# Optimization experiments

Hardware: AMD Instinct MI355X
Metric: run time of the kernel (lower is better)

Reference implementation:

```python
import jax, jax.numpy as jnp
import numpy as np

STATE_DIM = 512
HIDDEN = 256
ACTION = 8
BATCH = 32768
LN_EPS = 1e-5


def setup_inputs() -> dict:
    key = jax.random.key(0)
    ks = jax.random.split(key, 24)
    s = 0.02
    inp = {
        'initial_state': jax.random.normal(ks[0], (BATCH, STATE_DIM), jnp.float32),
        'final_state': jax.random.normal(ks[1], (BATCH, STATE_DIM), jnp.float32),
        'horizon': 10,
        # fc: Linear(1024->256), LayerNorm(256), ReLU, Linear(256->256), ReLU
        'W1': jax.random.normal(ks[2], (HIDDEN, 2 * STATE_DIM), jnp.float32) * s,
        'b1': jnp.zeros((HIDDEN,), jnp.float32),
        'ln_g': jnp.ones((HIDDEN,), jnp.float32),
        'ln_b': jnp.zeros((HIDDEN,), jnp.float32),
        'W2': jax.random.normal(ks[3], (HIDDEN, HIDDEN), jnp.float32) * s,
        'b2': jnp.zeros((HIDDEN,), jnp.float32),
        # GRU layer 0 (input=ACTION) and layer 1 (input=HIDDEN)
        'Wih0': jax.random.normal(ks[4], (3 * HIDDEN, ACTION), jnp.float32) * s,
        'Whh0': jax.random.normal(ks[5], (3 * HIDDEN, HIDDEN), jnp.float32) * s,
        'bih0': jnp.zeros((3 * HIDDEN,), jnp.float32),
        'bhh0': jnp.zeros((3 * HIDDEN,), jnp.float32),
        'Wih1': jax.random.normal(ks[6], (3 * HIDDEN, HIDDEN), jnp.float32) * s,
        'Whh1': jax.random.normal(ks[7], (3 * HIDDEN, HIDDEN), jnp.float32) * s,
        'bih1': jnp.zeros((3 * HIDDEN,), jnp.float32),
        'bhh1': jnp.zeros((3 * HIDDEN,), jnp.float32),
        # fc_action: 256 -> 8
        'Wa': jax.random.normal(ks[8], (ACTION, HIDDEN), jnp.float32) * s,
        'ba': jnp.zeros((ACTION,), jnp.float32),
        # fc_init_hidden: 256 -> 512
        'Winit': jax.random.normal(ks[9], (2 * HIDDEN, HIDDEN), jnp.float32) * s,
        'binit': jnp.zeros((2 * HIDDEN,), jnp.float32),
    }
    return inp


def _gru_cell(x, h, Wih, Whh, bih, bhh):
    # torch.nn.GRU cell: gates ordered [r, z, n]
    gi = x @ Wih.T + bih              # [B, 3H]
    gh = h @ Whh.T + bhh              # [B, 3H]
    i_r, i_z, i_n = jnp.split(gi, 3, axis=-1)
    h_r, h_z, h_n = jnp.split(gh, 3, axis=-1)
    r = jax.nn.sigmoid(i_r + h_r)
    z = jax.nn.sigmoid(i_z + h_z)
    n = jnp.tanh(i_n + r * h_n)
    return (1.0 - z) * n + z * h


def reference(initial_state, final_state, horizon, W1, b1, ln_g, ln_b, W2, b2,
              Wih0, Whh0, bih0, bhh0, Wih1, Whh1, bih1, bhh1, Wa, ba, Winit, binit):
    B = initial_state.shape[0]
    combined = jnp.concatenate([initial_state, final_state], axis=-1)  # [B, 2*state]
    h = combined @ W1.T + b1
    mu = jnp.mean(h, axis=-1, keepdims=True)
    var = jnp.var(h, axis=-1, keepdims=True)
    h = (h - mu) * jax.lax.rsqrt(var + LN_EPS) * ln_g + ln_b
    h = jax.nn.relu(h)
    h = jax.nn.relu(h @ W2.T + b2)    # [B, H]

    # Replicates torch .view(2, B, H) on a [B, 2H] tensor (row-major reshape)
    hidden = jnp.reshape(h @ Winit.T + binit, (2, B, HIDDEN))
    h0, h1 = hidden[0], hidden[1]
    a0 = jnp.zeros((B, ACTION), initial_state.dtype)

    def step(carry, _):
        h0, h1, a = carry
        h0n = _gru_cell(a, h0, Wih0, Whh0, bih0, bhh0)
        h1n = _gru_cell(h0n, h1, Wih1, Whh1, bih1, bhh1)
        logits = h1n @ Wa.T + ba       # [B, A]
        a_next = jax.nn.softmax(logits, axis=-1)
        return (h0n, h1n, a_next), logits

    _, logits_seq = jax.lax.scan(step, (h0, h1, a0), None, length=horizon)
    return jnp.transpose(logits_seq, (1, 0, 2))  # [B, horizon, A]
```

## Files before the change

### kernel.cpp

```cpp
#include <hip/hip_runtime.h>


#define HS 264

typedef __attribute__((ext_vector_type(8))) short short8;
typedef __attribute__((ext_vector_type(4))) float fvec4;

__device__ __forceinline__ float bf2f(unsigned short u) {
    union { unsigned int u; float f; } x; x.u = ((unsigned int)u) << 16; return x.f;
}
__device__ __forceinline__ unsigned short f2bf(float f) {
    union { float f; unsigned int u; } x; x.f = f;
    unsigned int r = x.u + 0x7fffu + ((x.u >> 16) & 1u);
    return (unsigned short)(r >> 16);
}
__device__ __forceinline__ float sigm(float x)   { return __builtin_amdgcn_rcpf(1.f + __expf(-x)); }
__device__ __forceinline__ float tanh_f(float x) { return 2.f * __builtin_amdgcn_rcpf(1.f + __expf(-2.f * x)) - 1.f; }

__device__ __forceinline__ short8 ld8(const unsigned short* p) {
    return *reinterpret_cast<const short8*>(p);
}
__device__ __forceinline__ fvec4 mfma16(short8 a, short8 b, fvec4 c) {
    return __builtin_amdgcn_mfma_f32_16x16x32_bf16(a, b, c, 0, 0, 0);
}
__device__ __forceinline__ fvec4 splat4(float v) {
    fvec4 r = {v, v, v, v}; return r;
}

__device__ __forceinline__ int packoff(int e, int K) {
    const int n = e / K, k = e % K;
    return (((n >> 4) * (K >> 5) + (k >> 5)) << 9)
         + (((((k >> 3) & 3) << 4) | (n & 15)) << 3) + (k & 7);
}

__global__ __launch_bounds__(256) void k_prep(
    const float* __restrict__ W1, const float* __restrict__ W2,
    const float* __restrict__ Winit, const float* __restrict__ Wih0,
    const float* __restrict__ Whh0, const float* __restrict__ Wih1,
    const float* __restrict__ Whh1, const float* __restrict__ Wa,
    unsigned short* __restrict__ wb)
{
    int i = blockIdx.x * 256 + threadIdx.x;
    if (i >= 1056768) return;
    float v; int dst;
    if (i < 262144) {
        v = W1[i];                dst = packoff(i, 1024);
    } else if (i < 327680) {
        int e = i - 262144;  v = W2[e];    dst = 262144 + packoff(e, 256);
    } else if (i < 458752) {
        int e = i - 327680;  v = Winit[e]; dst = 327680 + packoff(e, 256);
    } else if (i < 464896) {
        v = Wih0[i - 458752];     dst = i;
    } else if (i < 661504) {
        int e = i - 464896;  v = Whh0[e];  dst = 464896 + packoff(e, 256);
    } else if (i < 858112) {
        int e = i - 661504;  v = Wih1[e];  dst = 661504 + packoff(e, 256);
    } else if (i < 1054720) {
        int e = i - 858112;  v = Whh1[e];  dst = 858112 + packoff(e, 256);
    } else {
        v = Wa[i - 1054720];      dst = i;
    }
    wb[dst] = f2bf(v);
}

__global__ __launch_bounds__(512, 2) void k_encode(
    const float* __restrict__ ini, const float* __restrict__ fin,
    const unsigned short* __restrict__ W1b, const float* __restrict__ b1,
    const float* __restrict__ lng, const float* __restrict__ lnb,
    const unsigned short* __restrict__ W2b, const float* __restrict__ b2,
    const unsigned short* __restrict__ Winitb, const float* __restrict__ binit,
    unsigned short* __restrict__ h0g, unsigned short* __restrict__ h1g)
{
    __shared__ unsigned short hb[64 * HS];
    __shared__ unsigned short at[2][64 * 40];
    __shared__ float ps[64][8][2];
    __shared__ float st[64][2];
    const int tid = threadIdx.x, lane = tid & 63, w = tid >> 6;
    const int l15 = lane & 15, q = lane >> 4;
    const int rows0 = blockIdx.x * 64;
    const int c0 = w * 32;
    const fvec4 fz = {0.f, 0.f, 0.f, 0.f};

    const int srow = tid >> 3, sseg = (tid & 7) * 4;

    fvec4 acc[4][2];
#pragma unroll
    for (int rt = 0; rt < 4; ++rt) { acc[rt][0] = fz; acc[rt][1] = fz; }
    {
        const float* src0 = ini + (rows0 + srow) * 512 + sseg;
        fvec4 v = *reinterpret_cast<const fvec4*>(src0);
        union { unsigned short s[4]; unsigned long long u; } p;
        p.s[0] = f2bf(v[0]); p.s[1] = f2bf(v[1]); p.s[2] = f2bf(v[2]); p.s[3] = f2bf(v[3]);
        *reinterpret_cast<unsigned long long*>(&at[0][srow * 40 + sseg]) = p.u;
    }
    __syncthreads();
#pragma unroll 1
    for (int kc = 0; kc < 32; ++kc) {
        const int buf = kc & 1;
        if (kc < 31) {
            const int k0 = (kc + 1) * 32 + sseg;
            const float* src = (k0 < 512) ? (ini + (rows0 + srow) * 512 + k0)
                                          : (fin + (rows0 + srow) * 512 + (k0 - 512));
            fvec4 v = *reinterpret_cast<const fvec4*>(src);
            union { unsigned short s[4]; unsigned long long u; } p;
            p.s[0] = f2bf(v[0]); p.s[1] = f2bf(v[1]); p.s[2] = f2bf(v[2]); p.s[3] = f2bf(v[3]);
            *reinterpret_cast<unsigned long long*>(&at[buf ^ 1][srow * 40 + sseg]) = p.u;
        }
        short8 b8a = ld8(W1b + (((w * 2 + 0) * 32 + kc) * 64 + lane) * 8);
        short8 b8b = ld8(W1b + (((w * 2 + 1) * 32 + kc) * 64 + lane) * 8);
        short8 a8[4];
#pragma unroll
        for (int rt = 0; rt < 4; ++rt)
            a8[rt] = ld8(&at[buf][(rt * 16 + l15) * 40 + q * 8]);
#pragma unroll
        for (int rt = 0; rt < 4; ++rt) {
            acc[rt][0] = mfma16(a8[rt], b8a, acc[rt][0]);
            acc[rt][1] = mfma16(a8[rt], b8b, acc[rt][1]);
        }
        __syncthreads();
    }
    float bv[2] = { b1[c0 + l15], b1[c0 + 16 + l15] };
#pragma unroll
    for (int rt = 0; rt < 4; ++rt)
#pragma unroll
        for (int r = 0; r < 4; ++r) {
            float s = 0.f, s2 = 0.f;
#pragma unroll
            for (int ct = 0; ct < 2; ++ct) {
                float v = acc[rt][ct][r] + bv[ct];
                acc[rt][ct][r] = v;
                s += v; s2 += v * v;
            }
#pragma unroll
            for (int off = 1; off < 16; off <<= 1) {
                s  += __shfl_xor(s,  off, 64);
                s2 += __shfl_xor(s2, off, 64);
            }
            if (l15 == 0) {
                int row = rt * 16 + q * 4 + r;
                ps[row][w][0] = s; ps[row][w][1] = s2;
            }
        }
    __syncthreads();
    if (tid < 64) {
        float s = 0.f, s2 = 0.f;
#pragma unroll
        for (int j = 0; j < 8; ++j) { s += ps[tid][j][0]; s2 += ps[tid][j][1]; }
        float mu = s * (1.f / 256.f);
        float var = s2 * (1.f / 256.f) - mu * mu;
        st[tid][0] = mu; st[tid][1] = rsqrtf(var + 1e-5f);
    }
    __syncthreads();
    {
        float gv[2]  = { lng[c0 + l15], lng[c0 + 16 + l15] };
        float bbv[2] = { lnb[c0 + l15], lnb[c0 + 16 + l15] };
#pragma unroll
        for (int rt = 0; rt < 4; ++rt)
#pragma unroll
            for (int ct = 0; ct < 2; ++ct)
#pragma unroll
                for (int r = 0; r < 4; ++r) {
                    int row = rt * 16 + q * 4 + r;
                    float v = (acc[rt][ct][r] - st[row][0]) * st[row][1] * gv[ct] + bbv[ct];
                    v = fmaxf(v, 0.f);
                    hb[row * HS + c0 + ct * 16 + l15] = f2bf(v);
                }
    }
    __syncthreads();
    fvec4 acc2[4][2];
#pragma unroll
    for (int rt = 0; rt < 4; ++rt) { acc2[rt][0] = fz; acc2[rt][1] = fz; }
#pragma unroll 2
    for (int kc = 0; kc < 8; ++kc) {
        const int k0 = kc * 32 + q * 8;
        short8 a8[4];
#pragma unroll
        for (int rt = 0; rt < 4; ++rt) a8[rt] = ld8(hb + (rt * 16 + l15) * HS + k0);
#pragma unroll
        for (int ct = 0; ct < 2; ++ct) {
            short8 b8 = ld8(W2b + (((w * 2 + ct) * 8 + kc) * 64 + lane) * 8);
#pragma unroll
            for (int rt = 0; rt < 4; ++rt) acc2[rt][ct] = mfma16(a8[rt], b8, acc2[rt][ct]);
        }
    }
    {
        float b2v[2] = { b2[c0 + l15], b2[c0 + 16 + l15] };
        unsigned short stg[4][2][4];
#pragma unroll
        for (int rt = 0; rt < 4; ++rt)
#pragma unroll
            for (int ct = 0; ct < 2; ++ct)
#pragma unroll
                for (int r = 0; r < 4; ++r)
                    stg[rt][ct][r] = f2bf(fmaxf(acc2[rt][ct][r] + b2v[ct], 0.f));
        __syncthreads();
#pragma unroll
        for (int rt = 0; rt < 4; ++rt)
#pragma unroll
            for (int ct = 0; ct < 2; ++ct)
#pragma unroll
                for (int r = 0; r < 4; ++r)
                    hb[(rt * 16 + q * 4 + r) * HS + c0 + ct * 16 + l15] = stg[rt][ct][r];
    }
    __syncthreads();
    fvec4 a3[4][4];
#pragma unroll
    for (int rt = 0; rt < 4; ++rt)
#pragma unroll
        for (int ct = 0; ct < 4; ++ct) a3[rt][ct] = fz;
#pragma unroll 1
    for (int kc = 0; kc < 8; ++kc) {
        const int k0 = kc * 32 + q * 8;
        short8 a8[4];
#pragma unroll
        for (int rt = 0; rt < 4; ++rt) a8[rt] = ld8(hb + (rt * 16 + l15) * HS + k0);
#pragma unroll
        for (int ct = 0; ct < 4; ++ct) {
            short8 b8 = ld8(Winitb + (((w * 4 + ct) * 8 + kc) * 64 + lane) * 8);
#pragma unroll
            for (int rt = 0; rt < 4; ++rt) a3[rt][ct] = mfma16(a8[rt], b8, a3[rt][ct]);
        }
    }
    const int c0i = w * 64;
#pragma unroll
    for (int ct = 0; ct < 4; ++ct) {
        const int j = c0i + ct * 16 + l15;
        const float bz = binit[j];
        const int half = j >> 8, cc = j & 255;
#pragma unroll
        for (int rt = 0; rt < 4; ++rt)
#pragma unroll
            for (int r = 0; r < 4; ++r) {
                const int i = rows0 + rt * 16 + q * 4 + r;
                const unsigned short v = f2bf(a3[rt][ct][r] + bz);
                if (i < 16384) h0g[(2 * i + half) * 256 + cc] = v;
                else           h1g[(2 * (i - 16384) + half) * 256 + cc] = v;
            }
    }
}

__global__ __launch_bounds__(512, 2) void k_roll(
    const unsigned short* __restrict__ h0g, const unsigned short* __restrict__ h1g,
    const unsigned short* __restrict__ Wih0b, const unsigned short* __restrict__ Whh0b,
    const unsigned short* __restrict__ Wih1b, const unsigned short* __restrict__ Whh1b,
    const unsigned short* __restrict__ Wab,
    const float* __restrict__ bih0, const float* __restrict__ bhh0,
    const float* __restrict__ bih1, const float* __restrict__ bhh1,
    const float* __restrict__ ba, float* __restrict__ out)
{
    __shared__ unsigned short h0sb[2][64 * HS];
    __shared__ unsigned short h1sb[2][64 * HS];
    __shared__ unsigned short avs[64 * 8];
    __shared__ float ldsb[2048];
    const int tid = threadIdx.x, lane = tid & 63, w = tid >> 6;
    const int l15 = lane & 15, q = lane >> 4;
    const int rows0 = blockIdx.x * 64;
    const int cb = w * 32;
    const fvec4 fz = {0.f, 0.f, 0.f, 0.f};
    const short8 z8 = {0,0,0,0,0,0,0,0};

    for (int it = tid; it < 64 * 32; it += 512) {
        const int row = it >> 5, g = (it & 31) * 8;
        *reinterpret_cast<short8*>(&h0sb[0][row * HS + g]) = ld8(h0g + (rows0 + row) * 256 + g);
        *reinterpret_cast<short8*>(&h1sb[0][row * HS + g]) = ld8(h1g + (rows0 + row) * 256 + g);
    }
    if (tid < 256) {
        const int j = tid;
        ldsb[j]       = bih0[j] + bhh0[j];
        ldsb[256 + j] = bih0[256 + j] + bhh0[256 + j];
        ldsb[512 + j] = bih0[512 + j];
        ldsb[768 + j] = bhh0[512 + j];
    } else {
        const int j = tid - 256;
        ldsb[1024 + j] = bih1[j] + bhh1[j];
        ldsb[1280 + j] = bih1[256 + j] + bhh1[256 + j];
        ldsb[1536 + j] = bih1[512 + j];
        ldsb[1792 + j] = bhh1[512 + j];
    }
    const float bav = ba[l15 & 7];
    __syncthreads();

    for (int t = 0; t < 10; ++t) {
        const int cur = t & 1, nxt = cur ^ 1;
        const unsigned short* h0c = h0sb[cur];
        unsigned short*       h0n = h0sb[nxt];
        const unsigned short* h1c = h1sb[cur];
        unsigned short*       h1n = h1sb[nxt];
        {
            fvec4 aR[4][2], aZ[4][2], aNi[4][2], aNh[4][2];
#pragma unroll
            for (int ct = 0; ct < 2; ++ct) {
                const int c = cb + ct * 16 + l15;
                const float vr = ldsb[c],       vz = ldsb[256 + c];
                const float vi = ldsb[512 + c], vh = ldsb[768 + c];
#pragma unroll
                for (int rt = 0; rt < 4; ++rt) {
                    aR[rt][ct]  = splat4(vr);
                    aZ[rt][ct]  = splat4(vz);
                    aNi[rt][ct] = splat4(vi);
                    aNh[rt][ct] = splat4(vh);
                }
            }
#pragma unroll 2
            for (int kc = 0; kc < 8; ++kc) {
                const int k0 = kc * 32 + q * 8;
                short8 wr[2], wz[2], wn[2];
#pragma unroll
                for (int ct = 0; ct < 2; ++ct) {
                    const unsigned short* wp =
                        Whh0b + ((((w * 2 + ct) * 8 + kc) * 64 + lane) * 8);
                    wr[ct] = ld8(wp);
                    wz[ct] = ld8(wp + 65536);
                    wn[ct] = ld8(wp + 131072);
                }
                short8 ah[4];
#pragma unroll
                for (int rt = 0; rt < 4; ++rt)
                    ah[rt] = ld8(h0c + (rt * 16 + l15) * HS + k0);
#pragma unroll
                for (int ct = 0; ct < 2; ++ct)
#pragma unroll
                    for (int rt = 0; rt < 4; ++rt) {
                        aR[rt][ct]  = mfma16(ah[rt], wr[ct], aR[rt][ct]);
                        aZ[rt][ct]  = mfma16(ah[rt], wz[ct], aZ[rt][ct]);
                        aNh[rt][ct] = mfma16(ah[rt], wn[ct], aNh[rt][ct]);
                    }
            }
            if (t > 0) {
                short8 av[4];
#pragma unroll
                for (int rt = 0; rt < 4; ++rt) {
                    short8 v = ld8(avs + (rt * 16 + l15) * 8);
                    av[rt] = (q == 0) ? v : z8;
                }
#pragma unroll
                for (int ct = 0; ct < 2; ++ct) {
                    const unsigned short* wp = Wih0b + (cb + ct * 16 + l15) * 8;
                    short8 wr = ld8(wp);
                    short8 wz = ld8(wp + 2048);
                    short8 wn = ld8(wp + 4096);
#pragma unroll
                    for (int rt = 0; rt < 4; ++rt) {
                        aR[rt][ct]  = mfma16(av[rt], wr, aR[rt][ct]);
                        aZ[rt][ct]  = mfma16(av[rt], wz, aZ[rt][ct]);
                        aNi[rt][ct] = mfma16(av[rt], wn, aNi[rt][ct]);
                    }
                }
            }
#pragma unroll
            for (int ct = 0; ct < 2; ++ct) {
                const int c = cb + ct * 16 + l15;
#pragma unroll
                for (int rt = 0; rt < 4; ++rt)
#pragma unroll
                    for (int r = 0; r < 4; ++r) {
                        const int row = rt * 16 + q * 4 + r;
                        const float hold = bf2f(h0c[row * HS + c]);
                        const float rr = sigm(aR[rt][ct][r]);
                        const float zz = sigm(aZ[rt][ct][r]);
                        const float nn = tanh_f(aNi[rt][ct][r] + rr * aNh[rt][ct][r]);
                        h0n[row * HS + c] = f2bf((1.f - zz) * nn + zz * hold);
                    }
            }
        }
        __syncthreads();
        {
            fvec4 aR[4][2], aZ[4][2], aNi[4][2], aNh[4][2];
#pragma unroll
            for (int ct = 0; ct < 2; ++ct) {
                const int c = cb + ct * 16 + l15;
                const float vr = ldsb[1024 + c], vz = ldsb[1280 + c];
                const float vi = ldsb[1536 + c], vh = ldsb[1792 + c];
#pragma unroll
                for (int rt = 0; rt < 4; ++rt) {
                    aR[rt][ct]  = splat4(vr);
                    aZ[rt][ct]  = splat4(vz);
                    aNi[rt][ct] = splat4(vi);
                    aNh[rt][ct] = splat4(vh);
                }
            }
#pragma unroll 1
            for (int kc = 0; kc < 8; ++kc) {
                const int k0 = kc * 32 + q * 8;
                short8 wir[2], wiz[2], win[2], whr[2], whz[2], whn[2];
#pragma unroll
                for (int ct = 0; ct < 2; ++ct) {
                    const int fo = (((w * 2 + ct) * 8 + kc) * 64 + lane) * 8;
                    const unsigned short* wi = Wih1b + fo;
                    const unsigned short* wh = Whh1b + fo;
                    wir[ct] = ld8(wi);
                    whr[ct] = ld8(wh);
                    wiz[ct] = ld8(wi + 65536);
                    whz[ct] = ld8(wh + 65536);
                    win[ct] = ld8(wi + 131072);
                    whn[ct] = ld8(wh + 131072);
                }
                short8 ai[4], ah[4];
#pragma unroll
                for (int rt = 0; rt < 4; ++rt) {
                    const int rr = (rt * 16 + l15) * HS + k0;
                    ai[rt] = ld8(h0n + rr);
                    ah[rt] = ld8(h1c + rr);
                }
#pragma unroll
                for (int ct = 0; ct < 2; ++ct)
#pragma unroll
                    for (int rt = 0; rt < 4; ++rt) {
                        aR[rt][ct]  = mfma16(ai[rt], wir[ct], aR[rt][ct]);
                        aR[rt][ct]  = mfma16(ah[rt], whr[ct], aR[rt][ct]);
                        aZ[rt][ct]  = mfma16(ai[rt], wiz[ct], aZ[rt][ct]);
                        aZ[rt][ct]  = mfma16(ah[rt], whz[ct], aZ[rt][ct]);
                        aNi[rt][ct] = mfma16(ai[rt], win[ct], aNi[rt][ct]);
                        aNh[rt][ct] = mfma16(ah[rt], whn[ct], aNh[rt][ct]);
                    }
            }
#pragma unroll
            for (int ct = 0; ct < 2; ++ct) {
                const int c = cb + ct * 16 + l15;
#pragma unroll
                for (int rt = 0; rt < 4; ++rt)
#pragma unroll
                    for (int r = 0; r < 4; ++r) {
                        const int row = rt * 16 + q * 4 + r;
                        const float hold = bf2f(h1c[row * HS + c]);
                        const float rr = sigm(aR[rt][ct][r]);
                        const float zz = sigm(aZ[rt][ct][r]);
                        const float nn = tanh_f(aNi[rt][ct][r] + rr * aNh[rt][ct][r]);
                        h1n[row * HS + c] = f2bf((1.f - zz) * nn + zz * hold);
                    }
            }
        }
        __syncthreads();
        if (w < 4) {
            fvec4 f = fz;
#pragma unroll 1
            for (int kc = 0; kc < 8; ++kc) {
                const int k0 = kc * 32 + q * 8;
                short8 a8 = ld8(h1n + (w * 16 + l15) * HS + k0);
                short8 b8 = ld8(Wab + (l15 & 7) * 256 + k0);
                f = mfma16(a8, b8, f);
            }
#pragma unroll
            for (int r = 0; r < 4; ++r) {
                float s = f[r] + bav;
                float m = s;
                m = fmaxf(m, __shfl_xor(m, 1, 64));
                m = fmaxf(m, __shfl_xor(m, 2, 64));
                m = fmaxf(m, __shfl_xor(m, 4, 64));
                float e = __expf(s - m);
                float se = e;
                se += __shfl_xor(se, 1, 64);
                se += __shfl_xor(se, 2, 64);
                se += __shfl_xor(se, 4, 64);
                if (l15 < 8) {
                    const int lrow = w * 16 + q * 4 + r;
                    out[(rows0 + lrow) * 80 + t * 8 + l15] = s;
                    avs[lrow * 8 + l15] = f2bf(e * __builtin_amdgcn_rcpf(se));
                }
            }
        }
        __syncthreads();
    }
}

extern "C" void kernel_launch(void* const* d_in, const int* in_sizes, int n_in,
                              void* d_out, int out_size, void* d_ws, size_t ws_size,
                              hipStream_t stream)
{
    const float* ini   = (const float*)d_in[0];
    const float* fin   = (const float*)d_in[1];
    const float* W1    = (const float*)d_in[3];
    const float* b1    = (const float*)d_in[4];
    const float* lng   = (const float*)d_in[5];
    const float* lnb   = (const float*)d_in[6];
    const float* W2    = (const float*)d_in[7];
    const float* b2    = (const float*)d_in[8];
    const float* Wih0  = (const float*)d_in[9];
    const float* Whh0  = (const float*)d_in[10];
    const float* bih0  = (const float*)d_in[11];
    const float* bhh0  = (const float*)d_in[12];
    const float* Wih1  = (const float*)d_in[13];
    const float* Whh1  = (const float*)d_in[14];
    const float* bih1  = (const float*)d_in[15];
    const float* bhh1  = (const float*)d_in[16];
    const float* Wa    = (const float*)d_in[17];
    const float* ba    = (const float*)d_in[18];
    const float* Winit = (const float*)d_in[19];
    const float* binit = (const float*)d_in[20];
    float* out = (float*)d_out;

    char* ws = (char*)d_ws;
    unsigned short* wb     = (unsigned short*)ws;
    unsigned short* W1b    = wb;
    unsigned short* W2b    = wb + 262144;
    unsigned short* Winitb = wb + 327680;
    unsigned short* Wih0b  = wb + 458752;
    unsigned short* Whh0b  = wb + 464896;
    unsigned short* Wih1b  = wb + 661504;
    unsigned short* Whh1b  = wb + 858112;
    unsigned short* Wab    = wb + 1054720;
    unsigned short* h0g = (unsigned short*)(ws + 2113536);
    unsigned short* h1g = (unsigned short*)(ws + 18890752);

    k_prep<<<dim3(4128), dim3(256), 0, stream>>>(W1, W2, Winit, Wih0, Whh0, Wih1, Whh1, Wa, wb);
    k_encode<<<dim3(512), dim3(512), 0, stream>>>(ini, fin, W1b, b1, lng, lnb, W2b, b2,
                                                  Winitb, binit, h0g, h1g);
    k_roll<<<dim3(512), dim3(512), 0, stream>>>(h0g, h1g, Wih0b, Whh0b, Wih1b, Whh1b, Wab,
                                                bih0, bhh0, bih1, bhh1, ba, out);
}
```

Before: 701.0 us.

## Single-buffer GRU hidden state in LDS and process column tiles sequentially for occupancy

Replaces the double-buffered LDS hidden-state arrays with single buffers, staging each step's new h values packed in registers and writing them back after an extra barrier. The two column tiles per wave are now processed one after another with smaller accumulator arrays, and launch bounds are raised so four blocks can be resident per CU. This halves LDS use and cuts register pressure to allow more concurrent blocks, which should hide latency better. The cost is two extra __syncthreads per timestep and weight and h loads issued per column tile, with less instruction-level parallelism per wave.

```diff
diff --git a/kernel.cpp b/kernel.cpp
--- a/kernel.cpp
+++ b/kernel.cpp
@@ -239,7 +239,7 @@
     }
 }
 
-__global__ __launch_bounds__(512, 2) void k_roll(
+__global__ __launch_bounds__(512, 4) void k_roll(
     const unsigned short* __restrict__ h0g, const unsigned short* __restrict__ h1g,
     const unsigned short* __restrict__ Wih0b, const unsigned short* __restrict__ Whh0b,
     const unsigned short* __restrict__ Wih1b, const unsigned short* __restrict__ Whh1b,
@@ -248,8 +248,8 @@
     const float* __restrict__ bih1, const float* __restrict__ bhh1,
     const float* __restrict__ ba, float* __restrict__ out)
 {
-    __shared__ unsigned short h0sb[2][64 * HS];
-    __shared__ unsigned short h1sb[2][64 * HS];
+    __shared__ unsigned short h0s[64 * HS];
+    __shared__ unsigned short h1s[64 * HS];
     __shared__ unsigned short avs[64 * 8];
     __shared__ float ldsb[2048];
     const int tid = threadIdx.x, lane = tid & 63, w = tid >> 6;
@@ -261,8 +261,8 @@
 
     for (int it = tid; it < 64 * 32; it += 512) {
         const int row = it >> 5, g = (it & 31) * 8;
-        *reinterpret_cast<short8*>(&h0sb[0][row * HS + g]) = ld8(h0g + (rows0 + row) * 256 + g);
-        *reinterpret_cast<short8*>(&h1sb[0][row * HS + g]) = ld8(h1g + (rows0 + row) * 256 + g);
+        *reinterpret_cast<short8*>(&h0s[row * HS + g]) = ld8(h0g + (rows0 + row) * 256 + g);
+        *reinterpret_cast<short8*>(&h1s[row * HS + g]) = ld8(h1g + (rows0 + row) * 256 + g);
     }
     if (tid < 256) {
         const int j = tid;
@@ -281,162 +281,147 @@
     __syncthreads();
 
     for (int t = 0; t < 10; ++t) {
-        const int cur = t & 1, nxt = cur ^ 1;
-        const unsigned short* h0c = h0sb[cur];
-        unsigned short*       h0n = h0sb[nxt];
-        const unsigned short* h1c = h1sb[cur];
-        unsigned short*       h1n = h1sb[nxt];
-        {
-            fvec4 aR[4][2], aZ[4][2], aNi[4][2], aNh[4][2];
-#pragma unroll
-            for (int ct = 0; ct < 2; ++ct) {
-                const int c = cb + ct * 16 + l15;
+        unsigned int st0[16];
+#pragma unroll 1
+        for (int p = 0; p < 2; ++p) {
+            const int c = cb + p * 16 + l15;
+            fvec4 aR[4], aZ[4], aNi[4], aNh[4];
+            {
                 const float vr = ldsb[c],       vz = ldsb[256 + c];
                 const float vi = ldsb[512 + c], vh = ldsb[768 + c];
 #pragma unroll
                 for (int rt = 0; rt < 4; ++rt) {
-                    aR[rt][ct]  = splat4(vr);
-                    aZ[rt][ct]  = splat4(vz);
-                    aNi[rt][ct] = splat4(vi);
-                    aNh[rt][ct] = splat4(vh);
-                }
-            }
-#pragma unroll 2
+                    aR[rt]  = splat4(vr);
+                    aZ[rt]  = splat4(vz);
+                    aNi[rt] = splat4(vi);
+                    aNh[rt] = splat4(vh);
+                }
+            }
+#pragma unroll 1
             for (int kc = 0; kc < 8; ++kc) {
                 const int k0 = kc * 32 + q * 8;
-                short8 wr[2], wz[2], wn[2];
-#pragma unroll
-                for (int ct = 0; ct < 2; ++ct) {
-                    const unsigned short* wp =
-                        Whh0b + ((((w * 2 + ct) * 8 + kc) * 64 + lane) * 8);
-                    wr[ct] = ld8(wp);
-                    wz[ct] = ld8(wp + 65536);
-                    wn[ct] = ld8(wp + 131072);
-                }
-                short8 ah[4];
-#pragma unroll
-                for (int rt = 0; rt < 4; ++rt)
-                    ah[rt] = ld8(h0c + (rt * 16 + l15) * HS + k0);
-#pragma unroll
-                for (int ct = 0; ct < 2; ++ct)
-#pragma unroll
-                    for (int rt = 0; rt < 4; ++rt) {
-                        aR[rt][ct]  = mfma16(ah[rt], wr[ct], aR[rt][ct]);
-                        aZ[rt][ct]  = mfma16(ah[rt], wz[ct], aZ[rt][ct]);
-                        aNh[rt][ct] = mfma16(ah[rt], wn[ct], aNh[rt][ct]);
-                    }
+                const unsigned short* wp =
+                    Whh0b + ((((w * 2 + p) * 8 + kc) * 64 + lane) * 8);
+                const short8 wr = ld8(wp);
+                const short8 wz = ld8(wp + 65536);
+                const short8 wn = ld8(wp + 131072);
+#pragma unroll
+                for (int rt = 0; rt < 4; ++rt) {
+                    const short8 ah = ld8(h0s + (rt * 16 + l15) * HS + k0);
+                    aR[rt]  = mfma16(ah, wr, aR[rt]);
+                    aZ[rt]  = mfma16(ah, wz, aZ[rt]);
+                    aNh[rt] = mfma16(ah, wn, aNh[rt]);
+                }
             }
             if (t > 0) {
-                short8 av[4];
+                const unsigned short* wp = Wih0b + c * 8;
+                const short8 wr = ld8(wp);
+                const short8 wz = ld8(wp + 2048);
+                const short8 wn = ld8(wp + 4096);
 #pragma unroll
                 for (int rt = 0; rt < 4; ++rt) {
                     short8 v = ld8(avs + (rt * 16 + l15) * 8);
-                    av[rt] = (q == 0) ? v : z8;
-                }
-#pragma unroll
-                for (int ct = 0; ct < 2; ++ct) {
-                    const unsigned short* wp = Wih0b + (cb + ct * 16 + l15) * 8;
-                    short8 wr = ld8(wp);
-                    short8 wz = ld8(wp + 2048);
-                    short8 wn = ld8(wp + 4096);
-#pragma unroll
-                    for (int rt = 0; rt < 4; ++rt) {
-                        aR[rt][ct]  = mfma16(av[rt], wr, aR[rt][ct]);
-                        aZ[rt][ct]  = mfma16(av[rt], wz, aZ[rt][ct]);
-                        aNi[rt][ct] = mfma16(av[rt], wn, aNi[rt][ct]);
-                    }
-                }
-            }
-#pragma unroll
-            for (int ct = 0; ct < 2; ++ct) {
-                const int c = cb + ct * 16 + l15;
-#pragma unroll
-                for (int rt = 0; rt < 4; ++rt)
-#pragma unroll
-                    for (int r = 0; r < 4; ++r) {
-                        const int row = rt * 16 + q * 4 + r;
-                        const float hold = bf2f(h0c[row * HS + c]);
-                        const float rr = sigm(aR[rt][ct][r]);
-                        const float zz = sigm(aZ[rt][ct][r]);
-                        const float nn = tanh_f(aNi[rt][ct][r] + rr * aNh[rt][ct][r]);
-                        h0n[row * HS + c] = f2bf((1.f - zz) * nn + zz * hold);
-                    }
-            }
-        }
-        __syncthreads();
-        {
-            fvec4 aR[4][2], aZ[4][2], aNi[4][2], aNh[4][2];
-#pragma unroll
-            for (int ct = 0; ct < 2; ++ct) {
-                const int c = cb + ct * 16 + l15;
+                    const short8 av = (q == 0) ? v : z8;
+                    aR[rt]  = mfma16(av, wr, aR[rt]);
+                    aZ[rt]  = mfma16(av, wz, aZ[rt]);
+                    aNi[rt] = mfma16(av, wn, aNi[rt]);
+                }
+            }
+#pragma unroll
+            for (int rt = 0; rt < 4; ++rt)
+#pragma unroll
+                for (int r = 0; r < 4; ++r) {
+                    const int row = rt * 16 + q * 4 + r;
+                    const float hold = bf2f(h0s[row * HS + c]);
+                    const float rr = sigm(aR[rt][r]);
+                    const float zz = sigm(aZ[rt][r]);
+                    const float nn = tanh_f(aNi[rt][r] + rr * aNh[rt][r]);
+                    const unsigned int v = f2bf((1.f - zz) * nn + zz * hold);
+                    st0[rt * 4 + r] = p ? (st0[rt * 4 + r] | (v << 16)) : v;
+                }
+        }
+        __syncthreads();
+#pragma unroll
+        for (int rt = 0; rt < 4; ++rt)
+#pragma unroll
+            for (int r = 0; r < 4; ++r) {
+                const int row = rt * 16 + q * 4 + r;
+                const unsigned int v = st0[rt * 4 + r];
+                h0s[row * HS + cb + l15]      = (unsigned short)v;
+                h0s[row * HS + cb + 16 + l15] = (unsigned short)(v >> 16);
+            }
+        __syncthreads();
+        unsigned int st1[16];
+#pragma unroll 1
+        for (int p = 0; p < 2; ++p) {
+            const int c = cb + p * 16 + l15;
+            fvec4 aR[4], aZ[4], aNi[4], aNh[4];
+            {
                 const float vr = ldsb[1024 + c], vz = ldsb[1280 + c];
                 const float vi = ldsb[1536 + c], vh = ldsb[1792 + c];
 #pragma unroll
                 for (int rt = 0; rt < 4; ++rt) {
-                    aR[rt][ct]  = splat4(vr);
-                    aZ[rt][ct]  = splat4(vz);
-                    aNi[rt][ct] = splat4(vi);
-                    aNh[rt][ct] = splat4(vh);
+                    aR[rt]  = splat4(vr);
+                    aZ[rt]  = splat4(vz);
+                    aNi[rt] = splat4(vi);
+                    aNh[rt] = splat4(vh);
                 }
             }
 #pragma unroll 1
             for (int kc = 0; kc < 8; ++kc) {
                 const int k0 = kc * 32 + q * 8;
-                short8 wir[2], wiz[2], win[2], whr[2], whz[2], whn[2];
-#pragma unroll
-                for (int ct = 0; ct < 2; ++ct) {
-                    const int fo = (((w * 2 + ct) * 8 + kc) * 64 + lane) * 8;
-                    const unsigned short* wi = Wih1b + fo;
-                    const unsigned short* wh = Whh1b + fo;
-                    wir[ct] = ld8(wi);
-                    whr[ct] = ld8(wh);
-                    wiz[ct] = ld8(wi + 65536);
-                    whz[ct] = ld8(wh + 65536);
-                    win[ct] = ld8(wi + 131072);
-                    whn[ct] = ld8(wh + 131072);
-                }
-                short8 ai[4], ah[4];
+                const int fo = ((((w * 2 + p) * 8 + kc) * 64 + lane) * 8);
+                const unsigned short* wi = Wih1b + fo;
+                const unsigned short* wh = Whh1b + fo;
+                const short8 wir = ld8(wi);
+                const short8 whr = ld8(wh);
+                const short8 wiz = ld8(wi + 65536);
+                const short8 whz = ld8(wh + 65536);
+                const short8 win = ld8(wi + 131072);
+                const short8 whn = ld8(wh + 131072);
 #pragma unroll
                 for (int rt = 0; rt < 4; ++rt) {
-                    const int rr = (rt * 16 + l15) * HS + k0;
-                    ai[rt] = ld8(h0n + rr);
-                    ah[rt] = ld8(h1c + rr);
-                }
-#pragma unroll
-                for (int ct = 0; ct < 2; ++ct)
-#pragma unroll
-                    for (int rt = 0; rt < 4; ++rt) {
-                        aR[rt][ct]  = mfma16(ai[rt], wir[ct], aR[rt][ct]);
-                        aR[rt][ct]  = mfma16(ah[rt], whr[ct], aR[rt][ct]);
-                        aZ[rt][ct]  = mfma16(ai[rt], wiz[ct], aZ[rt][ct]);
-                        aZ[rt][ct]  = mfma16(ah[rt], whz[ct], aZ[rt][ct]);
-                        aNi[rt][ct] = mfma16(ai[rt], win[ct], aNi[rt][ct]);
-                        aNh[rt][ct] = mfma16(ah[rt], whn[ct], aNh[rt][ct]);
-                    }
-            }
-#pragma unroll
-            for (int ct = 0; ct < 2; ++ct) {
-                const int c = cb + ct * 16 + l15;
-#pragma unroll
-                for (int rt = 0; rt < 4; ++rt)
-#pragma unroll
-                    for (int r = 0; r < 4; ++r) {
-                        const int row = rt * 16 + q * 4 + r;
-                        const float hold = bf2f(h1c[row * HS + c]);
-                        const float rr = sigm(aR[rt][ct][r]);
-                        const float zz = sigm(aZ[rt][ct][r]);
-                        const float nn = tanh_f(aNi[rt][ct][r] + rr * aNh[rt][ct][r]);
-                        h1n[row * HS + c] = f2bf((1.f - zz) * nn + zz * hold);
-                    }
-            }
-        }
+                    const int ro = (rt * 16 + l15) * HS + k0;
+                    const short8 ai = ld8(h0s + ro);
+                    const short8 ah = ld8(h1s + ro);
+                    aR[rt]  = mfma16(ai, wir, aR[rt]);
+                    aR[rt]  = mfma16(ah, whr, aR[rt]);
+                    aZ[rt]  = mfma16(ai, wiz, aZ[rt]);
+                    aZ[rt]  = mfma16(ah, whz, aZ[rt]);
+                    aNi[rt] = mfma16(ai, win, aNi[rt]);
+                    aNh[rt] = mfma16(ah, whn, aNh[rt]);
+                }
+            }
+#pragma unroll
+            for (int rt = 0; rt < 4; ++rt)
+#pragma unroll
+                for (int r = 0; r < 4; ++r) {
+                    const int row = rt * 16 + q * 4 + r;
+                    const float hold = bf2f(h1s[row * HS + c]);
+                    const float rr = sigm(aR[rt][r]);
+                    const float zz = sigm(aZ[rt][r]);
+                    const float nn = tanh_f(aNi[rt][r] + rr * aNh[rt][r]);
+                    const unsigned int v = f2bf((1.f - zz) * nn + zz * hold);
+                    st1[rt * 4 + r] = p ? (st1[rt * 4 + r] | (v << 16)) : v;
+                }
+        }
+        __syncthreads();
+#pragma unroll
+        for (int rt = 0; rt < 4; ++rt)
+#pragma unroll
+            for (int r = 0; r < 4; ++r) {
+                const int row = rt * 16 + q * 4 + r;
+                const unsigned int v = st1[rt * 4 + r];
+                h1s[row * HS + cb + l15]      = (unsigned short)v;
+                h1s[row * HS + cb + 16 + l15] = (unsigned short)(v >> 16);
+            }
         __syncthreads();
         if (w < 4) {
             fvec4 f = fz;
 #pragma unroll 1
             for (int kc = 0; kc < 8; ++kc) {
                 const int k0 = kc * 32 + q * 8;
-                short8 a8 = ld8(h1n + (w * 16 + l15) * HS + k0);
+                short8 a8 = ld8(h1s + (w * 16 + l15) * HS + k0);
                 short8 b8 = ld8(Wab + (l15 & 7) * 256 + k0);
                 f = mfma16(a8, b8, f);
             }
```

Result: slower. 791.2 us (+12.9%).

## Swizzle GRU hidden-state LDS layout and split layer-1 input/hidden GEMM loops

Applied to the files above, without the earlier changes.

Replaces the padded LDS row stride (264) with an unpadded 256 stride plus an XOR swizzle on the k index, applied consistently to every read and write of the hidden-state buffers. The aim is to avoid bank conflicts and cut LDS footprint, which could allow better occupancy. The layer-1 GRU loop is split into separate input-weight and hidden-weight passes, each unrolled by 2, so fewer weight registers are live per iteration. The added swizzle arithmetic and the doubled loop overhead are the costs.

```diff
diff --git a/kernel.cpp b/kernel.cpp
--- a/kernel.cpp
+++ b/kernel.cpp
@@ -2,6 +2,7 @@
 
 
 #define HS 264
+#define HR 256
 
 typedef __attribute__((ext_vector_type(8))) short short8;
 typedef __attribute__((ext_vector_type(4))) float fvec4;
@@ -25,6 +26,9 @@
 }
 __device__ __forceinline__ fvec4 splat4(float v) {
     fvec4 r = {v, v, v, v}; return r;
+}
+__device__ __forceinline__ int swz(int row, int k) {
+    return row * HR + (k ^ ((row & 7) << 3));
 }
 
 __device__ __forceinline__ int packoff(int e, int K) {
@@ -248,8 +252,8 @@
     const float* __restrict__ bih1, const float* __restrict__ bhh1,
     const float* __restrict__ ba, float* __restrict__ out)
 {
-    __shared__ unsigned short h0sb[2][64 * HS];
-    __shared__ unsigned short h1sb[2][64 * HS];
+    __shared__ unsigned short h0sb[2][64 * HR];
+    __shared__ unsigned short h1sb[2][64 * HR];
     __shared__ unsigned short avs[64 * 8];
     __shared__ float ldsb[2048];
     const int tid = threadIdx.x, lane = tid & 63, w = tid >> 6;
@@ -261,8 +265,9 @@
 
     for (int it = tid; it < 64 * 32; it += 512) {
         const int row = it >> 5, g = (it & 31) * 8;
-        *reinterpret_cast<short8*>(&h0sb[0][row * HS + g]) = ld8(h0g + (rows0 + row) * 256 + g);
-        *reinterpret_cast<short8*>(&h1sb[0][row * HS + g]) = ld8(h1g + (rows0 + row) * 256 + g);
+        const int d = swz(row, g);
+        *reinterpret_cast<short8*>(&h0sb[0][d]) = ld8(h0g + (rows0 + row) * 256 + g);
+        *reinterpret_cast<short8*>(&h1sb[0][d]) = ld8(h1g + (rows0 + row) * 256 + g);
     }
     if (tid < 256) {
         const int j = tid;
@@ -316,7 +321,7 @@
                 short8 ah[4];
 #pragma unroll
                 for (int rt = 0; rt < 4; ++rt)
-                    ah[rt] = ld8(h0c + (rt * 16 + l15) * HS + k0);
+                    ah[rt] = ld8(h0c + swz(rt * 16 + l15, k0));
 #pragma unroll
                 for (int ct = 0; ct < 2; ++ct)
 #pragma unroll
@@ -355,11 +360,11 @@
 #pragma unroll
                     for (int r = 0; r < 4; ++r) {
                         const int row = rt * 16 + q * 4 + r;
-                        const float hold = bf2f(h0c[row * HS + c]);
+                        const float hold = bf2f(h0c[swz(row, c)]);
                         const float rr = sigm(aR[rt][ct][r]);
                         const float zz = sigm(aZ[rt][ct][r]);
                         const float nn = tanh_f(aNi[rt][ct][r] + rr * aNh[rt][ct][r]);
-                        h0n[row * HS + c] = f2bf((1.f - zz) * nn + zz * hold);
+                        h0n[swz(row, c)] = f2bf((1.f - zz) * nn + zz * hold);
                     }
             }
         }
@@ -379,38 +384,53 @@
                     aNh[rt][ct] = splat4(vh);
                 }
             }
-#pragma unroll 1
+#pragma unroll 2
             for (int kc = 0; kc < 8; ++kc) {
                 const int k0 = kc * 32 + q * 8;
-                short8 wir[2], wiz[2], win[2], whr[2], whz[2], whn[2];
+                short8 wir[2], wiz[2], win[2];
 #pragma unroll
                 for (int ct = 0; ct < 2; ++ct) {
-                    const int fo = (((w * 2 + ct) * 8 + kc) * 64 + lane) * 8;
-                    const unsigned short* wi = Wih1b + fo;
-                    const unsigned short* wh = Whh1b + fo;
+                    const unsigned short* wi =
+                        Wih1b + ((((w * 2 + ct) * 8 + kc) * 64 + lane) * 8);
                     wir[ct] = ld8(wi);
-                    whr[ct] = ld8(wh);
                     wiz[ct] = ld8(wi + 65536);
-                    whz[ct] = ld8(wh + 65536);
                     win[ct] = ld8(wi + 131072);
-                    whn[ct] = ld8(wh + 131072);
-                }
-                short8 ai[4], ah[4];
-#pragma unroll
-                for (int rt = 0; rt < 4; ++rt) {
-                    const int rr = (rt * 16 + l15) * HS + k0;
-                    ai[rt] = ld8(h0n + rr);
-                    ah[rt] = ld8(h1c + rr);
-                }
+                }
+                short8 ai[4];
+#pragma unroll
+                for (int rt = 0; rt < 4; ++rt)
+                    ai[rt] = ld8(h0n + swz(rt * 16 + l15, k0));
 #pragma unroll
                 for (int ct = 0; ct < 2; ++ct)
 #pragma unroll
                     for (int rt = 0; rt < 4; ++rt) {
                         aR[rt][ct]  = mfma16(ai[rt], wir[ct], aR[rt][ct]);
+                        aZ[rt][ct]  = mfma16(ai[rt], wiz[ct], aZ[rt][ct]);
+                        aNi[rt][ct] = mfma16(ai[rt], win[ct], aNi[rt][ct]);
+                    }
+            }
+#pragma unroll 2
+            for (int kc = 0; kc < 8; ++kc) {
+                const int k0 = kc * 32 + q * 8;
+                short8 whr[2], whz[2], whn[2];
+#pragma unroll
+                for (int ct = 0; ct < 2; ++ct) {
+                    const unsigned short* wh =
+                        Whh1b + ((((w * 2 + ct) * 8 + kc) * 64 + lane) * 8);
+                    whr[ct] = ld8(wh);
+                    whz[ct] = ld8(wh + 65536);
+                    whn[ct] = ld8(wh + 131072);
+                }
+                short8 ah[4];
+#pragma unroll
+                for (int rt = 0; rt < 4; ++rt)
+                    ah[rt] = ld8(h1c + swz(rt * 16 + l15, k0));
+#pragma unroll
+                for (int ct = 0; ct < 2; ++ct)
+#pragma unroll
+                    for (int rt = 0; rt < 4; ++rt) {
                         aR[rt][ct]  = mfma16(ah[rt], whr[ct], aR[rt][ct]);
-                        aZ[rt][ct]  = mfma16(ai[rt], wiz[ct], aZ[rt][ct]);
                         aZ[rt][ct]  = mfma16(ah[rt], whz[ct], aZ[rt][ct]);
-                        aNi[rt][ct] = mfma16(ai[rt], win[ct], aNi[rt][ct]);
                         aNh[rt][ct] = mfma16(ah[rt], whn[ct], aNh[rt][ct]);
                     }
             }
@@ -422,11 +442,11 @@
 #pragma unroll
                     for (int r = 0; r < 4; ++r) {
                         const int row = rt * 16 + q * 4 + r;
-                        const float hold = bf2f(h1c[row * HS + c]);
+                        const float hold = bf2f(h1c[swz(row, c)]);
                         const float rr = sigm(aR[rt][ct][r]);
                         const float zz = sigm(aZ[rt][ct][r]);
                         const float nn = tanh_f(aNi[rt][ct][r] + rr * aNh[rt][ct][r]);
-                        h1n[row * HS + c] = f2bf((1.f - zz) * nn + zz * hold);
+                        h1n[swz(row, c)] = f2bf((1.f - zz) * nn + zz * hold);
                     }
             }
         }
@@ -436,7 +456,7 @@
 #pragma unroll 1
             for (int kc = 0; kc < 8; ++kc) {
                 const int k0 = kc * 32 + q * 8;
-                short8 a8 = ld8(h1n + (w * 16 + l15) * HS + k0);
+                short8 a8 = ld8(h1n + swz(w * 16 + l15, k0));
                 short8 b8 = ld8(Wab + (l15 & 7) * 256 + k0);
                 f = mfma16(a8, b8, f);
             }
```

Result: no change. 702.9 us (+0.3%).
